# Kernel tuning notes

Measured on AMD Instinct MI355X. Metric: run time of the kernel, lower is better.

Reference implementation:

```python
import jax, jax.numpy as jnp
import numpy as np

NUM_HEADS = 4
GROUPS = 8          # min(8, ch) with ch=256
EPS = 1e-5          # torch GroupNorm default eps


def setup_inputs() -> dict:
    key = jax.random.key(0)
    ks = jax.random.split(key, 3)
    b, c, h, w = 8, 256, 32, 32
    x = jax.random.normal(ks[0], (b, c, h, w), jnp.float32)
    gn_gamma = jnp.ones((c,), jnp.float32)
    gn_beta = jnp.zeros((c,), jnp.float32)
    qkv_w = jax.random.normal(ks[1], (3 * c, c), jnp.float32) * (c ** -0.5)
    qkv_b = jnp.zeros((3 * c,), jnp.float32)
    proj_w = jax.random.normal(ks[2], (c, c), jnp.float32) * (c ** -0.5)
    proj_b = jnp.zeros((c,), jnp.float32)
    return {"x": x, "gn_gamma": gn_gamma, "gn_beta": gn_beta,
            "qkv_w": qkv_w, "qkv_b": qkv_b, "proj_w": proj_w, "proj_b": proj_b}


def _group_norm(x, gamma, beta):
    b, c, h, w = x.shape
    xg = x.reshape(b, GROUPS, c // GROUPS, h, w)
    mean = xg.mean(axis=(2, 3, 4), keepdims=True)
    var = xg.var(axis=(2, 3, 4), keepdims=True)
    xn = ((xg - mean) * jax.lax.rsqrt(var + EPS)).reshape(b, c, h, w)
    return xn * gamma[None, :, None, None] + beta[None, :, None, None]


def reference(x, gn_gamma, gn_beta, qkv_w, qkv_b, proj_w, proj_b):
    b, c, h, w = x.shape
    dh = c // NUM_HEADS
    xn = _group_norm(x, gn_gamma, gn_beta)
    # 1x1 conv == channel matmul
    qkv = jnp.einsum('oc,bchw->bohw', qkv_w, xn) + qkv_b[None, :, None, None]
    qkv = qkv.reshape(b, 3, NUM_HEADS, dh, h * w)
    q, k, v = qkv[:, 0], qkv[:, 1], qkv[:, 2]   # each (b, n, dh, hw)
    scale = dh ** -0.5
    # full (hw x hw) attention matrix, matching the original explicit einsum
    attn = jax.nn.softmax(jnp.einsum('bncd,bnce->bnde', q, k) * scale, axis=-1)
    out = jnp.einsum('bnde,bnce->bncd', attn, v).reshape(b, c, h, w)
    out = jnp.einsum('oc,bchw->bohw', proj_w, out) + proj_b[None, :, None, None]
    return x + out
```

## Files before the change

kernel.cpp:

```cpp
#include <hip/hip_runtime.h>
#include <stdint.h>

typedef __attribute__((ext_vector_type(8))) short short8;
typedef __attribute__((ext_vector_type(4))) float f32x4;

#define BB 8
#define CC 256
#define PP 1024
#define NH 4
#define DH 64

__device__ __forceinline__ unsigned short f2bf(float f) {
  union { float f; unsigned u; } v; v.f = f;
  unsigned r = v.u + 0x7FFFu + ((v.u >> 16) & 1u);
  return (unsigned short)(r >> 16);
}

__device__ __forceinline__ float bf2f(unsigned short u) {
  union { unsigned u; float f; } v; v.u = ((unsigned)u) << 16;
  return v.f;
}

__device__ __forceinline__ f32x4 mfma16(short8 a, short8 b, f32x4 c) {
  return __builtin_amdgcn_mfma_f32_16x16x32_bf16(a, b, c, 0, 0, 0);
}

__global__ __launch_bounds__(256) void prep(
    const float* __restrict__ x, float2* __restrict__ part,
    const float* __restrict__ qkvw, const float* __restrict__ projw,
    unsigned short* __restrict__ wall) {
  int blk = blockIdx.x;
  int tid = threadIdx.x;
  if (blk < 512) {
    int sl = blk & 7, g = (blk >> 3) & 7, b = blk >> 6;
    const float4* xb =
        (const float4*)(x + (size_t)(b * CC + g * 32) * PP) + sl * 1024;
    float s = 0.f, q = 0.f;
    for (int i = tid; i < 1024; i += 256) {
      float4 v = xb[i];
      s += v.x + v.y + v.z + v.w;
      q += v.x * v.x + v.y * v.y + v.z * v.z + v.w * v.w;
    }
    for (int off = 32; off > 0; off >>= 1) {
      s += __shfl_down(s, off);
      q += __shfl_down(q, off);
    }
    __shared__ float rs[4], rq[4];
    int w = tid >> 6;
    if ((tid & 63) == 0) { rs[w] = s; rq[w] = q; }
    __syncthreads();
    if (tid == 0)
      part[blk] = make_float2(rs[0] + rs[1] + rs[2] + rs[3],
                              rq[0] + rq[1] + rq[2] + rq[3]);
  } else {
    int i4 = (blk - 512) * 256 + tid;
    float4 v = (i4 < 49152) ? ((const float4*)qkvw)[i4]
                            : ((const float4*)projw)[i4 - 49152];
    ushort4 o;
    o.x = f2bf(v.x); o.y = f2bf(v.y); o.z = f2bf(v.z); o.w = f2bf(v.w);
    ((ushort4*)wall)[i4] = o;
  }
}

__global__ __launch_bounds__(256) void norm_t(
    const float* __restrict__ x, const float2* __restrict__ part,
    const float* __restrict__ gamma, const float* __restrict__ beta,
    unsigned short* __restrict__ xnT) {
  int p0 = blockIdx.x * 64, c0 = blockIdx.y * 64, b = blockIdx.z;
  int tid = threadIdx.x;
  __shared__ float ms[2], rstd[2];
  __shared__ unsigned short T[64][72];
  if (tid < 2) {
    int g = blockIdx.y * 2 + tid;
    float S = 0.f, Q = 0.f;
    for (int i = 0; i < 8; ++i) {
      float2 pp = part[b * 64 + g * 8 + i];
      S += pp.x; Q += pp.y;
    }
    float mean = S * (1.f / 32768.f);
    float var = Q * (1.f / 32768.f) - mean * mean;
    ms[tid] = mean;
    rstd[tid] = rsqrtf(var + 1e-5f);
  }
  __syncthreads();
  for (int it = 0; it < 4; ++it) {
    int l = tid + 256 * it;
    int cc = l >> 4, p4 = l & 15;
    int c = c0 + cc, gi = cc >> 5;
    float sc = rstd[gi] * gamma[c];
    float sh = beta[c] - ms[gi] * sc;
    float4 v = *(const float4*)(x + (size_t)(b * CC + c) * PP + p0 + p4 * 4);
    T[p4 * 4 + 0][cc] = f2bf(v.x * sc + sh);
    T[p4 * 4 + 1][cc] = f2bf(v.y * sc + sh);
    T[p4 * 4 + 2][cc] = f2bf(v.z * sc + sh);
    T[p4 * 4 + 3][cc] = f2bf(v.w * sc + sh);
  }
  __syncthreads();
  for (int it = 0; it < 2; ++it) {
    int l = tid + 256 * it;
    int p = l >> 3, seg = l & 7;
    *(short8*)(xnT + ((size_t)b * PP + p0 + p) * CC + c0 + seg * 8) =
        *(const short8*)&T[p][seg * 8];
  }
}

__global__ __launch_bounds__(256) void qkv_gemm(
    const unsigned short* __restrict__ xnT, const unsigned short* __restrict__ wbf,
    const float* __restrict__ qkvb, unsigned short* __restrict__ qb,
    unsigned short* __restrict__ kb, unsigned short* __restrict__ vT) {
  int p0 = blockIdx.x * 128, o0 = blockIdx.y * 128, b = blockIdx.z;
  int tid = threadIdx.x;
  int w = tid >> 6, lane = tid & 63, lq = lane >> 4, ln = lane & 15;
  int wy = w >> 1, wx = w & 1;
  __shared__ unsigned short A_l[128][40];
  __shared__ unsigned short B_l[128][40];
  f32x4 acc[4][4];
  for (int i = 0; i < 4; ++i)
    for (int j = 0; j < 4; ++j) acc[i][j] = (f32x4){0.f, 0.f, 0.f, 0.f};
  for (int kc = 0; kc < 256; kc += 32) {
    for (int it = 0; it < 2; ++it) {
      int l = tid + 256 * it;
      int row = l >> 2, seg = l & 3;
      *(short8*)&A_l[row][seg * 8] =
          *(const short8*)(xnT + ((size_t)b * PP + p0 + row) * CC + kc + seg * 8);
      *(short8*)&B_l[row][seg * 8] =
          *(const short8*)(wbf + (size_t)(o0 + row) * CC + kc + seg * 8);
    }
    __syncthreads();
    short8 af[4], bf[4];
    for (int i = 0; i < 4; ++i)
      af[i] = *(const short8*)&A_l[wy * 64 + i * 16 + ln][lq * 8];
    for (int j = 0; j < 4; ++j)
      bf[j] = *(const short8*)&B_l[wx * 64 + j * 16 + ln][lq * 8];
    for (int i = 0; i < 4; ++i)
      for (int j = 0; j < 4; ++j) acc[i][j] = mfma16(af[i], bf[j], acc[i][j]);
    __syncthreads();
  }
  for (int i = 0; i < 4; ++i) {
    for (int j = 0; j < 4; ++j) {
      int o = o0 + wx * 64 + j * 16 + ln;
      int s = o >> 8, h = (o >> 6) & 3, ch = o & 63;
      float bias = qkvb[o];
      float mul = (s == 0) ? 0.125f : 1.0f;
      size_t bh = (size_t)b * NH + h;
      for (int r = 0; r < 4; ++r) {
        int p = p0 + wy * 64 + i * 16 + lq * 4 + r;
        unsigned short val = f2bf((acc[i][j][r] + bias) * mul);
        if (s == 2) {
          vT[(bh * DH + ch) * PP + p] = val;
        } else {
          unsigned short* dst = (s == 0) ? qb : kb;
          dst[(bh * PP + p) * DH + ch] = val;
        }
      }
    }
  }
}

__global__ __launch_bounds__(256) void attn(
    const unsigned short* __restrict__ qb, const unsigned short* __restrict__ kb,
    const unsigned short* __restrict__ vT, unsigned short* __restrict__ attnT) {
  int d0 = blockIdx.x * 64, h = blockIdx.y, b = blockIdx.z;
  int tid = threadIdx.x;
  int w = tid >> 6, lane = tid & 63, lq = lane >> 4, ln = lane & 15;
  size_t bh = (size_t)b * NH + h;
  const unsigned short* qbase = qb + bh * PP * DH;
  const unsigned short* kbase = kb + bh * PP * DH;
  const unsigned short* vbase = vT + bh * DH * PP;

  __shared__ __align__(16) char SM[53248];
  unsigned short (*K_l)[72] = (unsigned short (*)[72])(SM);
  unsigned short (*V_l)[136] = (unsigned short (*)[136])(SM + 18432);
  unsigned short (*P_l)[136] = (unsigned short (*)[136])(SM + 35840);
  unsigned short* Obf = (unsigned short*)(SM);
  float* lsums = (float*)(SM + 36864);

  int ke = tid >> 1, kseg = tid & 1;
  int vch = tid >> 2, vseg = tid & 3;

  short8 qf[4][2];
#pragma unroll
  for (int ds = 0; ds < 4; ++ds)
#pragma unroll
    for (int kc = 0; kc < 2; ++kc)
      qf[ds][kc] = *(const short8*)(qbase + (size_t)(d0 + ds * 16 + ln) * DH +
                                    kc * 32 + lq * 8);

  float lsum[4] = {0.f, 0.f, 0.f, 0.f};
  f32x4 o_acc[4][4];
#pragma unroll
  for (int i = 0; i < 4; ++i)
#pragma unroll
    for (int j = 0; j < 4; ++j) o_acc[i][j] = (f32x4){0.f, 0.f, 0.f, 0.f};

  short8 kr[4], vr[4];
#pragma unroll
  for (int i = 0; i < 4; ++i)
    kr[i] = *(const short8*)(kbase + (size_t)ke * DH + kseg * 32 + i * 8);
#pragma unroll
  for (int i = 0; i < 4; ++i)
    vr[i] = *(const short8*)(vbase + (size_t)vch * PP + vseg * 32 + i * 8);

  for (int e0 = 0; e0 < PP; e0 += 128) {
#pragma unroll
    for (int i = 0; i < 4; ++i)
      *(short8*)&K_l[ke][kseg * 32 + i * 8] = kr[i];
#pragma unroll
    for (int i = 0; i < 4; ++i)
      *(short8*)&V_l[vch][vseg * 32 + i * 8] = vr[i];
    if (e0 + 128 < PP) {
      int en = e0 + 128;
#pragma unroll
      for (int i = 0; i < 4; ++i)
        kr[i] = *(const short8*)(kbase + (size_t)(en + ke) * DH + kseg * 32 + i * 8);
#pragma unroll
      for (int i = 0; i < 4; ++i)
        vr[i] = *(const short8*)(vbase + (size_t)vch * PP + en + vseg * 32 + i * 8);
    }
    __syncthreads();
#pragma unroll
    for (int es = 0; es < 2; ++es) {
      short8 ka0 = *(const short8*)&K_l[w * 32 + es * 16 + ln][lq * 8];
      short8 ka1 = *(const short8*)&K_l[w * 32 + es * 16 + ln][32 + lq * 8];
      f32x4 sc[4];
#pragma unroll
      for (int ds = 0; ds < 4; ++ds) {
        f32x4 a = (f32x4){0.f, 0.f, 0.f, 0.f};
        a = mfma16(ka0, qf[ds][0], a);
        a = mfma16(ka1, qf[ds][1], a);
        sc[ds] = a;
      }
#pragma unroll
      for (int ds = 0; ds < 4; ++ds) {
        float p0 = __expf(fminf(sc[ds][0], 60.f));
        float p1 = __expf(fminf(sc[ds][1], 60.f));
        float p2 = __expf(fminf(sc[ds][2], 60.f));
        float p3 = __expf(fminf(sc[ds][3], 60.f));
        lsum[ds] += (p0 + p1) + (p2 + p3);
        union { unsigned short u[4]; unsigned long long ll; } pk;
        pk.u[0] = f2bf(p0); pk.u[1] = f2bf(p1);
        pk.u[2] = f2bf(p2); pk.u[3] = f2bf(p3);
        *(unsigned long long*)&P_l[ds * 16 + ln][w * 32 + es * 16 + lq * 4] =
            pk.ll;
      }
    }
    short8 pb[4];
#pragma unroll
    for (int ds = 0; ds < 4; ++ds)
      pb[ds] = *(const short8*)&P_l[ds * 16 + ln][w * 32 + lq * 8];
#pragma unroll
    for (int cs = 0; cs < 4; ++cs) {
      short8 va = *(const short8*)&V_l[cs * 16 + ln][w * 32 + lq * 8];
#pragma unroll
      for (int ds = 0; ds < 4; ++ds)
        o_acc[cs][ds] = mfma16(va, pb[ds], o_acc[cs][ds]);
    }
    __syncthreads();
  }
#pragma unroll
  for (int ds = 0; ds < 4; ++ds) {
    float s = lsum[ds];
    s += __shfl_xor(s, 16);
    s += __shfl_xor(s, 32);
    if (lq == 0) lsums[w * 64 + ds * 16 + ln] = s;
  }
#pragma unroll
  for (int cs = 0; cs < 4; ++cs) {
#pragma unroll
    for (int ds = 0; ds < 4; ++ds) {
      union { unsigned short u[4]; unsigned long long ll; } pk;
#pragma unroll
      for (int r = 0; r < 4; ++r) pk.u[r] = f2bf(o_acc[cs][ds][r]);
      *(unsigned long long*)&Obf[((w * 64 + ds * 16 + ln) * 72) + cs * 16 +
                                 lq * 4] = pk.ll;
    }
  }
  __syncthreads();
  {
    int d = tid >> 2, cr = tid & 3;
    float inv = 1.f / (lsums[d] + lsums[64 + d] + lsums[128 + d] + lsums[192 + d]);
    float o[16];
#pragma unroll
    for (int j = 0; j < 16; ++j) o[j] = 0.f;
#pragma unroll
    for (int ww = 0; ww < 4; ++ww) {
#pragma unroll
      for (int jj = 0; jj < 4; ++jj) {
        unsigned long long v = *(const unsigned long long*)&Obf[
            ((ww * 64 + d) * 72) + cr * 16 + jj * 4];
#pragma unroll
        for (int r = 0; r < 4; ++r)
          o[jj * 4 + r] += bf2f((unsigned short)(v >> (16 * r)));
      }
    }
    union { unsigned short u[16]; short8 s[2]; } pk;
#pragma unroll
    for (int j = 0; j < 16; ++j) pk.u[j] = f2bf(o[j] * inv);
    unsigned short* dst =
        attnT + ((size_t)b * PP + d0 + d) * CC + h * DH + cr * 16;
    *(short8*)dst = pk.s[0];
    *(short8*)(dst + 8) = pk.s[1];
  }
}

__global__ __launch_bounds__(256) void proj_gemm(
    const unsigned short* __restrict__ attnT, const unsigned short* __restrict__ pwbf,
    const float* __restrict__ projb, const float* __restrict__ x,
    float* __restrict__ out) {
  int p0 = blockIdx.x * 128, o0 = blockIdx.y * 64, b = blockIdx.z;
  int tid = threadIdx.x;
  int w = tid >> 6, lane = tid & 63, lq = lane >> 4, ln = lane & 15;
  __shared__ unsigned short A_l[64][40];
  __shared__ unsigned short B_l[128][40];
  f32x4 acc[4][2];
  for (int i = 0; i < 4; ++i)
    for (int j = 0; j < 2; ++j) acc[i][j] = (f32x4){0.f, 0.f, 0.f, 0.f};
  for (int kc = 0; kc < 256; kc += 32) {
    {
      int row = tid >> 2, seg = tid & 3;
      *(short8*)&A_l[row][seg * 8] =
          *(const short8*)(pwbf + (size_t)(o0 + row) * CC + kc + seg * 8);
    }
    for (int it = 0; it < 2; ++it) {
      int l = tid + 256 * it;
      int row = l >> 2, seg = l & 3;
      *(short8*)&B_l[row][seg * 8] =
          *(const short8*)(attnT + ((size_t)b * PP + p0 + row) * CC + kc + seg * 8);
    }
    __syncthreads();
    short8 af[4], bfr[2];
    for (int i = 0; i < 4; ++i)
      af[i] = *(const short8*)&A_l[i * 16 + ln][lq * 8];
    for (int j = 0; j < 2; ++j)
      bfr[j] = *(const short8*)&B_l[w * 32 + j * 16 + ln][lq * 8];
    for (int i = 0; i < 4; ++i)
      for (int j = 0; j < 2; ++j) acc[i][j] = mfma16(af[i], bfr[j], acc[i][j]);
    __syncthreads();
  }
  for (int i = 0; i < 4; ++i) {
    for (int j = 0; j < 2; ++j) {
      int p = p0 + w * 32 + j * 16 + ln;
      for (int r = 0; r < 4; ++r) {
        int o = o0 + i * 16 + lq * 4 + r;
        size_t idx = ((size_t)b * CC + o) * PP + p;
        out[idx] = x[idx] + projb[o] + acc[i][j][r];
      }
    }
  }
}

extern "C" void kernel_launch(void* const* d_in, const int* in_sizes, int n_in,
                              void* d_out, int out_size, void* d_ws, size_t ws_size,
                              hipStream_t stream) {
  const float* x = (const float*)d_in[0];
  const float* gamma = (const float*)d_in[1];
  const float* beta = (const float*)d_in[2];
  const float* qkvw = (const float*)d_in[3];
  const float* qkvb = (const float*)d_in[4];
  const float* projw = (const float*)d_in[5];
  const float* projb = (const float*)d_in[6];
  float* out = (float*)d_out;
  char* ws = (char*)d_ws;

  float2* part = (float2*)(ws + 0);
  unsigned short* xnT = (unsigned short*)(ws + 16384);
  unsigned short* wall = (unsigned short*)(ws + 4210688);
  unsigned short* pwbf = wall + 768 * 256;
  unsigned short* qb = (unsigned short*)(ws + 4734976);
  unsigned short* kb = (unsigned short*)(ws + 8929280);
  unsigned short* vT = (unsigned short*)(ws + 13123584);
  unsigned short* attnT = (unsigned short*)(ws + 17317888);

  prep<<<768, 256, 0, stream>>>(x, part, qkvw, projw, wall);
  norm_t<<<dim3(16, 4, 8), 256, 0, stream>>>(x, part, gamma, beta, xnT);
  qkv_gemm<<<dim3(8, 6, 8), 256, 0, stream>>>(xnT, wall, qkvb, qb, kb, vT);
  attn<<<dim3(16, 4, 8), 256, 0, stream>>>(qb, kb, vT, attnT);
  proj_gemm<<<dim3(8, 4, 8), 256, 0, stream>>>(attnT, pwbf, projb, x, out);
}
```

Baseline: 125.3 us.

## Split attention keys across waves with direct global K/V fragment loads

The attention kernel now handles 32 query positions per block instead of 64, doubling the grid to 1024 blocks. Each wave owns a disjoint quarter of the keys and loads K and V MFMA fragments straight from global memory, dropping the shared-memory K/V staging and the per-tile block barriers. Partial outputs are reduced across waves through LDS at the end, and launch bounds request 4 blocks per CU. This aims for higher occupancy and fewer syncs, at the cost of more redundant global K/V traffic (each block rereads all of K/V for half as many queries) and uncoalesced, unprefetched loads.

```diff
diff --git a/kernel.cpp b/kernel.cpp
--- a/kernel.cpp
+++ b/kernel.cpp
@@ -157,10 +157,10 @@
   }
 }
 
-__global__ __launch_bounds__(256) void attn(
+__global__ __launch_bounds__(256, 4) void attn(
     const unsigned short* __restrict__ qb, const unsigned short* __restrict__ kb,
     const unsigned short* __restrict__ vT, unsigned short* __restrict__ attnT) {
-  int d0 = blockIdx.x * 64, h = blockIdx.y, b = blockIdx.z;
+  int d0 = blockIdx.x * 32, h = blockIdx.y, b = blockIdx.z;
   int tid = threadIdx.x;
   int w = tid >> 6, lane = tid & 63, lq = lane >> 4, ln = lane & 15;
   size_t bh = (size_t)b * NH + h;
@@ -168,138 +168,110 @@
   const unsigned short* kbase = kb + bh * PP * DH;
   const unsigned short* vbase = vT + bh * DH * PP;
 
-  __shared__ __align__(16) char SM[53248];
-  unsigned short (*K_l)[72] = (unsigned short (*)[72])(SM);
-  unsigned short (*V_l)[136] = (unsigned short (*)[136])(SM + 18432);
-  unsigned short (*P_l)[136] = (unsigned short (*)[136])(SM + 35840);
-  unsigned short* Obf = (unsigned short*)(SM);
-  float* lsums = (float*)(SM + 36864);
-
-  int ke = tid >> 1, kseg = tid & 1;
-  int vch = tid >> 2, vseg = tid & 3;
-
-  short8 qf[4][2];
-#pragma unroll
-  for (int ds = 0; ds < 4; ++ds)
+  __shared__ __align__(16) char SM[18944];
+  unsigned short* P_l = (unsigned short*)(SM + w * 2560);
+  unsigned short* Obf = (unsigned short*)SM;
+  float* lsums = (float*)(SM + 18432);
+
+  short8 qf[2][2];
+#pragma unroll
+  for (int ds = 0; ds < 2; ++ds)
 #pragma unroll
     for (int kc = 0; kc < 2; ++kc)
       qf[ds][kc] = *(const short8*)(qbase + (size_t)(d0 + ds * 16 + ln) * DH +
                                     kc * 32 + lq * 8);
 
-  float lsum[4] = {0.f, 0.f, 0.f, 0.f};
-  f32x4 o_acc[4][4];
+  float lsum[2] = {0.f, 0.f};
+  f32x4 o_acc[4][2];
 #pragma unroll
   for (int i = 0; i < 4; ++i)
 #pragma unroll
-    for (int j = 0; j < 4; ++j) o_acc[i][j] = (f32x4){0.f, 0.f, 0.f, 0.f};
-
-  short8 kr[4], vr[4];
-#pragma unroll
-  for (int i = 0; i < 4; ++i)
-    kr[i] = *(const short8*)(kbase + (size_t)ke * DH + kseg * 32 + i * 8);
-#pragma unroll
-  for (int i = 0; i < 4; ++i)
-    vr[i] = *(const short8*)(vbase + (size_t)vch * PP + vseg * 32 + i * 8);
-
-  for (int e0 = 0; e0 < PP; e0 += 128) {
-#pragma unroll
-    for (int i = 0; i < 4; ++i)
-      *(short8*)&K_l[ke][kseg * 32 + i * 8] = kr[i];
-#pragma unroll
-    for (int i = 0; i < 4; ++i)
-      *(short8*)&V_l[vch][vseg * 32 + i * 8] = vr[i];
-    if (e0 + 128 < PP) {
-      int en = e0 + 128;
-#pragma unroll
-      for (int i = 0; i < 4; ++i)
-        kr[i] = *(const short8*)(kbase + (size_t)(en + ke) * DH + kseg * 32 + i * 8);
-#pragma unroll
-      for (int i = 0; i < 4; ++i)
-        vr[i] = *(const short8*)(vbase + (size_t)vch * PP + en + vseg * 32 + i * 8);
-    }
-    __syncthreads();
-#pragma unroll
-    for (int es = 0; es < 2; ++es) {
-      short8 ka0 = *(const short8*)&K_l[w * 32 + es * 16 + ln][lq * 8];
-      short8 ka1 = *(const short8*)&K_l[w * 32 + es * 16 + ln][32 + lq * 8];
-      f32x4 sc[4];
-#pragma unroll
-      for (int ds = 0; ds < 4; ++ds) {
+    for (int j = 0; j < 2; ++j) o_acc[i][j] = (f32x4){0.f, 0.f, 0.f, 0.f};
+
+  for (int sub = 0; sub < 8; ++sub) {
+    int e0 = w * 256 + sub * 32;
+    short8 kf[2][2], vf[4];
+#pragma unroll
+    for (int es = 0; es < 2; ++es)
+#pragma unroll
+      for (int kc = 0; kc < 2; ++kc)
+        kf[es][kc] = *(const short8*)(kbase + (size_t)(e0 + es * 16 + ln) * DH +
+                                      kc * 32 + lq * 8);
+#pragma unroll
+    for (int cs = 0; cs < 4; ++cs)
+      vf[cs] = *(const short8*)(vbase + (size_t)(cs * 16 + ln) * PP + e0 + lq * 8);
+    f32x4 sc[2][2];
+#pragma unroll
+    for (int es = 0; es < 2; ++es)
+#pragma unroll
+      for (int ds = 0; ds < 2; ++ds) {
         f32x4 a = (f32x4){0.f, 0.f, 0.f, 0.f};
-        a = mfma16(ka0, qf[ds][0], a);
-        a = mfma16(ka1, qf[ds][1], a);
-        sc[ds] = a;
+        a = mfma16(kf[es][0], qf[ds][0], a);
+        a = mfma16(kf[es][1], qf[ds][1], a);
+        sc[es][ds] = a;
       }
 #pragma unroll
-      for (int ds = 0; ds < 4; ++ds) {
-        float p0 = __expf(fminf(sc[ds][0], 60.f));
-        float p1 = __expf(fminf(sc[ds][1], 60.f));
-        float p2 = __expf(fminf(sc[ds][2], 60.f));
-        float p3 = __expf(fminf(sc[ds][3], 60.f));
+    for (int es = 0; es < 2; ++es)
+#pragma unroll
+      for (int ds = 0; ds < 2; ++ds) {
+        float p0 = __expf(fminf(sc[es][ds][0], 60.f));
+        float p1 = __expf(fminf(sc[es][ds][1], 60.f));
+        float p2 = __expf(fminf(sc[es][ds][2], 60.f));
+        float p3 = __expf(fminf(sc[es][ds][3], 60.f));
         lsum[ds] += (p0 + p1) + (p2 + p3);
         union { unsigned short u[4]; unsigned long long ll; } pk;
         pk.u[0] = f2bf(p0); pk.u[1] = f2bf(p1);
         pk.u[2] = f2bf(p2); pk.u[3] = f2bf(p3);
-        *(unsigned long long*)&P_l[ds * 16 + ln][w * 32 + es * 16 + lq * 4] =
+        *(unsigned long long*)&P_l[(ds * 16 + ln) * 40 + es * 16 + lq * 4] =
             pk.ll;
       }
-    }
-    short8 pb[4];
-#pragma unroll
-    for (int ds = 0; ds < 4; ++ds)
-      pb[ds] = *(const short8*)&P_l[ds * 16 + ln][w * 32 + lq * 8];
-#pragma unroll
-    for (int cs = 0; cs < 4; ++cs) {
-      short8 va = *(const short8*)&V_l[cs * 16 + ln][w * 32 + lq * 8];
-#pragma unroll
-      for (int ds = 0; ds < 4; ++ds)
-        o_acc[cs][ds] = mfma16(va, pb[ds], o_acc[cs][ds]);
-    }
-    __syncthreads();
-  }
-#pragma unroll
-  for (int ds = 0; ds < 4; ++ds) {
+    short8 pb[2];
+#pragma unroll
+    for (int ds = 0; ds < 2; ++ds)
+      pb[ds] = *(const short8*)&P_l[(ds * 16 + ln) * 40 + lq * 8];
+#pragma unroll
+    for (int cs = 0; cs < 4; ++cs)
+#pragma unroll
+      for (int ds = 0; ds < 2; ++ds)
+        o_acc[cs][ds] = mfma16(vf[cs], pb[ds], o_acc[cs][ds]);
+  }
+  __syncthreads();
+#pragma unroll
+  for (int ds = 0; ds < 2; ++ds) {
     float s = lsum[ds];
     s += __shfl_xor(s, 16);
     s += __shfl_xor(s, 32);
-    if (lq == 0) lsums[w * 64 + ds * 16 + ln] = s;
-  }
-#pragma unroll
-  for (int cs = 0; cs < 4; ++cs) {
-#pragma unroll
-    for (int ds = 0; ds < 4; ++ds) {
+    if (lq == 0) lsums[w * 32 + ds * 16 + ln] = s;
+  }
+#pragma unroll
+  for (int cs = 0; cs < 4; ++cs)
+#pragma unroll
+    for (int ds = 0; ds < 2; ++ds) {
       union { unsigned short u[4]; unsigned long long ll; } pk;
 #pragma unroll
       for (int r = 0; r < 4; ++r) pk.u[r] = f2bf(o_acc[cs][ds][r]);
-      *(unsigned long long*)&Obf[((w * 64 + ds * 16 + ln) * 72) + cs * 16 +
+      *(unsigned long long*)&Obf[(w * 32 + ds * 16 + ln) * 72 + cs * 16 +
                                  lq * 4] = pk.ll;
     }
-  }
   __syncthreads();
   {
-    int d = tid >> 2, cr = tid & 3;
-    float inv = 1.f / (lsums[d] + lsums[64 + d] + lsums[128 + d] + lsums[192 + d]);
-    float o[16];
-#pragma unroll
-    for (int j = 0; j < 16; ++j) o[j] = 0.f;
+    int d = tid >> 3, cseg = tid & 7;
+    float inv =
+        1.f / (lsums[d] + lsums[32 + d] + lsums[64 + d] + lsums[96 + d]);
+    float o[8];
+#pragma unroll
+    for (int j = 0; j < 8; ++j) o[j] = 0.f;
 #pragma unroll
     for (int ww = 0; ww < 4; ++ww) {
-#pragma unroll
-      for (int jj = 0; jj < 4; ++jj) {
-        unsigned long long v = *(const unsigned long long*)&Obf[
-            ((ww * 64 + d) * 72) + cr * 16 + jj * 4];
-#pragma unroll
-        for (int r = 0; r < 4; ++r)
-          o[jj * 4 + r] += bf2f((unsigned short)(v >> (16 * r)));
-      }
-    }
-    union { unsigned short u[16]; short8 s[2]; } pk;
-#pragma unroll
-    for (int j = 0; j < 16; ++j) pk.u[j] = f2bf(o[j] * inv);
-    unsigned short* dst =
-        attnT + ((size_t)b * PP + d0 + d) * CC + h * DH + cr * 16;
-    *(short8*)dst = pk.s[0];
-    *(short8*)(dst + 8) = pk.s[1];
+      short8 vv = *(const short8*)&Obf[(ww * 32 + d) * 72 + cseg * 8];
+#pragma unroll
+      for (int r = 0; r < 8; ++r) o[r] += bf2f((unsigned short)vv[r]);
+    }
+    union { unsigned short u[8]; short8 s; } pk;
+#pragma unroll
+    for (int j = 0; j < 8; ++j) pk.u[j] = f2bf(o[j] * inv);
+    *(short8*)(attnT + ((size_t)b * PP + d0 + d) * CC + h * DH + cseg * 8) =
+        pk.s;
   }
 }
 
@@ -374,6 +346,6 @@
   prep<<<768, 256, 0, stream>>>(x, part, qkvw, projw, wall);
   norm_t<<<dim3(16, 4, 8), 256, 0, stream>>>(x, part, gamma, beta, xnT);
   qkv_gemm<<<dim3(8, 6, 8), 256, 0, stream>>>(xnT, wall, qkvb, qb, kb, vT);
-  attn<<<dim3(16, 4, 8), 256, 0, stream>>>(qb, kb, vT, attnT);
+  attn<<<dim3(32, 4, 8), 256, 0, stream>>>(qb, kb, vT, attnT);
   proj_gemm<<<dim3(8, 4, 8), 256, 0, stream>>>(attnT, pwbf, projb, x, out);
 }
```

Measured after the change: 135.7 us. +8.3%, slower.
